# Kernel optimization log

Measured on AMD Instinct MI355X. Metric: run time of the kernel, lower is better.

## Reference

```python
import jax, jax.numpy as jnp
import numpy as np

B, OUT, IN = 2048, 4096, 4096
KEEPRATE = 0.5  # mid-training drop schedule state; first-call default masks nothing


def setup_inputs() -> dict:
    key = jax.random.key(0)
    k1, k2, k3, k4 = jax.random.split(key, 4)
    data = jax.random.normal(k1, (B, IN), dtype=jnp.float32)
    # weight parameter = fftn of a real N(0, 0.1) matrix, stored as complex
    w0 = jax.random.normal(k2, (OUT, IN), dtype=jnp.float32) * 0.1
    wc = jnp.fft.fftn(w0.astype(jnp.float32))
    w_real = jnp.real(wc).astype(jnp.float32)
    w_imag = jnp.imag(wc).astype(jnp.float32)
    bias = jax.random.normal(k3, (OUT,), dtype=jnp.float32) * 0.1
    # ZMAT: rank assignment, a permutation of 0..OUT*IN-1
    zmat = jax.random.permutation(k4, jnp.arange(OUT * IN, dtype=jnp.int64)).reshape(OUT, IN)
    return {"data": data, "w_real": w_real, "w_imag": w_imag, "bias": bias, "zmat": zmat}


def reference(data, w_real, w_imag, bias, zmat):
    O, I = w_real.shape
    numel = O * I
    threval = KEEPRATE * numel
    # IDROP: keep entries whose rank <= threshold (ZMAT > threval -> 0)
    idrop = (zmat.astype(jnp.float32) <= threval).astype(w_real.dtype)
    dropweight = (w_real + 1j * w_imag) * idrop  # masked FFT-domain weight
    # torch.fft.irfftn(dropweight, s=(O, I)): full ifft on dim 0, real irfft on dim 1
    # (numpy/jax irfft crops the last axis to I//2+1, same as torch)
    w_spatial = jnp.fft.irfftn(dropweight, s=(O, I), axes=(0, 1)).astype(data.dtype)
    return data @ w_spatial.T + bias
```

## Files before the change

### kernel.cpp

```cpp
#include <hip/hip_runtime.h>
#include <hip/hip_bf16.h>
#include <stdint.h>

#define OUT_N 4096
#define IN_N  4096
#define BATCH 2048
#define KHALF 2049

typedef __bf16 bf16x8 __attribute__((ext_vector_type(8)));
typedef float  f32x4  __attribute__((ext_vector_type(4)));

__device__ __forceinline__ unsigned short f2bf(float f) {
  unsigned int u = __builtin_bit_cast(unsigned int, f);
  u += 0x7FFFu + ((u >> 16) & 1u);
  return (unsigned short)(u >> 16);
}

__device__ __forceinline__ float2 cmul(float2 a, float2 b) {
  return make_float2(a.x * b.x - a.y * b.y, a.x * b.y + a.y * b.x);
}
__device__ __forceinline__ float2 cadd(float2 a, float2 b) { return make_float2(a.x + b.x, a.y + b.y); }
__device__ __forceinline__ float2 csub(float2 a, float2 b) { return make_float2(a.x - b.x, a.y - b.y); }
__device__ __forceinline__ float2 muli(float2 a) { return make_float2(-a.y, a.x); }

__device__ __forceinline__ void dft4i(float2& x0, float2& x1, float2& x2, float2& x3) {
  float2 t0 = cadd(x0, x2), t1 = csub(x0, x2);
  float2 t2 = cadd(x1, x3), t3 = csub(x1, x3);
  float2 it3 = muli(t3);
  x0 = cadd(t0, t2); x2 = csub(t0, t2);
  x1 = cadd(t1, it3); x3 = csub(t1, it3);
}

#define C8f  0.70710678118654752f
#define C16f 0.92387953251128676f
#define S16f 0.38268343236508977f

__device__ __forceinline__ void dft16i(float2 r[16]) {
  float2 t[16];
#pragma unroll
  for (int b = 0; b < 4; ++b) {
    float2 a0 = r[b], a1 = r[4 + b], a2 = r[8 + b], a3 = r[12 + b];
    dft4i(a0, a1, a2, a3);
    t[b * 4 + 0] = a0; t[b * 4 + 1] = a1; t[b * 4 + 2] = a2; t[b * 4 + 3] = a3;
  }
  const float2 W1 = make_float2(C16f, S16f);
  const float2 W2 = make_float2(C8f, C8f);
  const float2 W3 = make_float2(S16f, C16f);
  const float2 W6 = make_float2(-C8f, C8f);
  const float2 W9 = make_float2(-C16f, -S16f);
  t[5]  = cmul(t[5],  W1);  t[6]  = cmul(t[6],  W2);  t[7]  = cmul(t[7],  W3);
  t[9]  = cmul(t[9],  W2);  t[10] = muli(t[10]);      t[11] = cmul(t[11], W6);
  t[13] = cmul(t[13], W3);  t[14] = cmul(t[14], W6);  t[15] = cmul(t[15], W9);
#pragma unroll
  for (int q = 0; q < 4; ++q) {
    float2 a0 = t[q], a1 = t[4 + q], a2 = t[8 + q], a3 = t[12 + q];
    dft4i(a0, a1, a2, a3);
    r[q] = a0; r[q + 4] = a1; r[q + 8] = a2; r[q + 12] = a3;
  }
}

__device__ __forceinline__ void twiddle16(float2 r[16], float theta) {
  float sn, cs;
  __sincosf(theta, &sn, &cs);
  float2 w = make_float2(cs, sn);
  float2 wk = w;
  r[1] = cmul(r[1], wk);
#pragma unroll
  for (int k = 2; k < 16; ++k) {
    wk = cmul(wk, w);
    r[k] = cmul(r[k], wk);
  }
}

__device__ void fft4096_core(float2 r[16], float2* lds, int t) {
  dft16i(r);
  twiddle16(r, 1.53398078788564123e-3f * (float)t);
#pragma unroll
  for (int k1 = 0; k1 < 16; ++k1) lds[k1 * 257 + t] = r[k1];
  __syncthreads();
  const int k1 = t & 15, b = t >> 4;
  float2 s[16];
#pragma unroll
  for (int a = 0; a < 16; ++a) s[a] = lds[k1 * 257 + 16 * a + b];
  __syncthreads();
  dft16i(s);
  twiddle16(s, 2.45436926061702596e-2f * (float)b);
#pragma unroll
  for (int c = 0; c < 16; ++c) lds[k1 * 273 + c * 17 + b] = s[c];
  __syncthreads();
#pragma unroll
  for (int bb = 0; bb < 16; ++bb) r[bb] = lds[k1 * 273 + b * 17 + bb];
  dft16i(r);
}

__global__ void mask_transpose(const float* __restrict__ wr, const float* __restrict__ wi,
                               const int* __restrict__ zmat, float2* __restrict__ wt) {
  __shared__ float2 tile[32][33];
  const int k0 = blockIdx.x * 32;
  const int o0 = blockIdx.y * 32;
  const int tx = threadIdx.x;
  const int ty = threadIdx.y;
#pragma unroll
  for (int r = 0; r < 4; ++r) {
    int o = o0 + ty + r * 8;
    int k = k0 + tx;
    float2 v = make_float2(0.f, 0.f);
    if (k < KHALF) {
      size_t idx = (size_t)o * IN_N + k;
      if (zmat[idx] <= 8388608) v = make_float2(wr[idx], wi[idx]);
    }
    tile[ty + r * 8][tx] = v;
  }
  __syncthreads();
#pragma unroll
  for (int r = 0; r < 4; ++r) {
    int k = k0 + ty + r * 8;
    int o = o0 + tx;
    if (k < KHALF) wt[(size_t)k * OUT_N + o] = tile[tx][ty + r * 8];
  }
}

__global__ __launch_bounds__(256) void col_ifft(float2* __restrict__ wt) {
  __shared__ float2 lds[4368];
  const int t = threadIdx.x;
  float2* row = wt + (size_t)blockIdx.x * OUT_N;
  float2 r[16];
#pragma unroll
  for (int n1 = 0; n1 < 16; ++n1) r[n1] = row[n1 * 256 + t];
  fft4096_core(r, lds, t);
#pragma unroll
  for (int d = 0; d < 16; ++d) row[t + 256 * d] = r[d];
}

__global__ void transpose_ko(const float2* __restrict__ yt, float2* __restrict__ y) {
  __shared__ float2 tile[32][33];
  const int k0 = blockIdx.x * 32;
  const int o0 = blockIdx.y * 32;
  const int tx = threadIdx.x;
  const int ty = threadIdx.y;
#pragma unroll
  for (int r = 0; r < 4; ++r) {
    int k = k0 + ty + r * 8;
    int o = o0 + tx;
    if (k < KHALF) tile[ty + r * 8][tx] = yt[(size_t)k * OUT_N + o];
  }
  __syncthreads();
#pragma unroll
  for (int r = 0; r < 4; ++r) {
    int o = o0 + ty + r * 8;
    int k = k0 + tx;
    if (k < KHALF) y[(size_t)o * KHALF + k] = tile[tx][ty + r * 8];
  }
}

__global__ __launch_bounds__(256) void row_irfft(const float2* __restrict__ y,
                                                 unsigned short* __restrict__ wbf) {
  __shared__ float2 lds[4368];
  const int t = threadIdx.x;
  const float2* row = y + (size_t)blockIdx.x * KHALF;
#pragma unroll
  for (int j = 0; j < 9; ++j) {
    int k = t + j * 256;
    if (k < KHALF) lds[k] = row[k];
  }
  __syncthreads();
  float2 r[16];
#pragma unroll
  for (int n1 = 0; n1 < 16; ++n1) {
    int m = n1 * 256 + t;
    float2 v;
    if (m == 0)         v = make_float2(lds[0].x, 0.f);
    else if (m < 2048)  v = lds[m];
    else if (m == 2048) v = make_float2(lds[2048].x, 0.f);
    else { float2 u = lds[4096 - m]; v = make_float2(u.x, -u.y); }
    r[n1] = v;
  }
  __syncthreads();
  fft4096_core(r, lds, t);
  const float sc = 1.0f / (4096.0f * 4096.0f);
  unsigned short* orow = wbf + (size_t)blockIdx.x * IN_N;
#pragma unroll
  for (int d = 0; d < 16; ++d) orow[t + 256 * d] = f2bf(r[d].x * sc);
}

__global__ void cvt_bf16(const float* __restrict__ x, unsigned short* __restrict__ o, int n4) {
  int i = blockIdx.x * blockDim.x + threadIdx.x;
  if (i < n4) {
    float4 v = ((const float4*)x)[i];
    ushort4 r;
    r.x = f2bf(v.x); r.y = f2bf(v.y); r.z = f2bf(v.z); r.w = f2bf(v.w);
    ((ushort4*)o)[i] = r;
  }
}

__device__ __forceinline__ void gload_lds16(const void* gp, void* lp) {
  typedef const __attribute__((address_space(1))) void* gptr_t;
  typedef __attribute__((address_space(3))) void* lptr_t;
  __builtin_amdgcn_global_load_lds((gptr_t)(unsigned long long)gp,
                                   (lptr_t)(unsigned int)(unsigned long long)lp,
                                   16, 0, 0);
}

__global__ __launch_bounds__(256) void gemm_bt_bias(const unsigned short* __restrict__ A,
                                                    const unsigned short* __restrict__ B,
                                                    const float* __restrict__ bias,
                                                    float* __restrict__ C) {
  __shared__ __align__(16) unsigned short As[128 * 32];
  __shared__ __align__(16) unsigned short Bs[128 * 32];
  const int tid  = threadIdx.x;
  const int wave = tid >> 6;
  const int lane = tid & 63;
  const int gm0 = blockIdx.y * 128;
  const int gn0 = blockIdx.x * 128;

  f32x4 acc[4][4] = {};
  const int wm = wave >> 1, wn = wave & 1;
  const int lrow = lane >> 2;
  const int lcol = (lane & 3) * 8;

  for (int kt = 0; kt < IN_N; kt += 32) {
#pragma unroll
    for (int j = 0; j < 2; ++j) {
      const int rbase = wave * 32 + j * 16;
      gload_lds16(A + ((size_t)(gm0 + rbase + lrow) * IN_N + kt + lcol),
                  As + (size_t)rbase * 32);
      gload_lds16(B + ((size_t)(gn0 + rbase + lrow) * IN_N + kt + lcol),
                  Bs + (size_t)rbase * 32);
    }
    __syncthreads();

    bf16x8 af[4], bfr[4];
#pragma unroll
    for (int i = 0; i < 4; ++i) {
      af[i]  = *(const bf16x8*)&As[(wm * 64 + i * 16 + (lane & 15)) * 32 + (lane >> 4) * 8];
      bfr[i] = *(const bf16x8*)&Bs[(wn * 64 + i * 16 + (lane & 15)) * 32 + (lane >> 4) * 8];
    }
#pragma unroll
    for (int mi = 0; mi < 4; ++mi)
#pragma unroll
      for (int ni = 0; ni < 4; ++ni)
        acc[mi][ni] = __builtin_amdgcn_mfma_f32_16x16x32_bf16(af[mi], bfr[ni], acc[mi][ni], 0, 0, 0);
    __syncthreads();
  }

  const int col0 = gn0 + wn * 64 + (lane & 15);
  const int row0 = gm0 + wm * 64 + (lane >> 4) * 4;
#pragma unroll
  for (int mi = 0; mi < 4; ++mi) {
#pragma unroll
    for (int ni = 0; ni < 4; ++ni) {
      int col = col0 + ni * 16;
      float bv = bias[col];
#pragma unroll
      for (int r = 0; r < 4; ++r) {
        int row = row0 + mi * 16 + r;
        C[(size_t)row * OUT_N + col] = acc[mi][ni][r] + bv;
      }
    }
  }
}

extern "C" void kernel_launch(void* const* d_in, const int* in_sizes, int n_in,
                              void* d_out, int out_size, void* d_ws, size_t ws_size,
                              hipStream_t stream) {
  const float* data = (const float*)d_in[0];
  const float* wr   = (const float*)d_in[1];
  const float* wi   = (const float*)d_in[2];
  const float* bias = (const float*)d_in[3];
  const int*   zmat = (const int*)d_in[4];

  char* ws = (char*)d_ws;
  float2* wt = (float2*)ws;
  float2* y  = (float2*)(ws + 67141632ull);
  unsigned short* wbf = (unsigned short*)ws;
  unsigned short* dbf = (unsigned short*)(ws + 33554432ull);

  hipLaunchKernelGGL(mask_transpose, dim3(65, 128), dim3(32, 8), 0, stream, wr, wi, zmat, wt);
  hipLaunchKernelGGL(col_ifft,       dim3(2049),    dim3(256),   0, stream, wt);
  hipLaunchKernelGGL(transpose_ko,   dim3(65, 128), dim3(32, 8), 0, stream, wt, y);
  hipLaunchKernelGGL(row_irfft,      dim3(4096),    dim3(256),   0, stream, y, wbf);
  hipLaunchKernelGGL(cvt_bf16,       dim3(8192),    dim3(256),   0, stream, data, dbf, (BATCH * IN_N) / 4);
  hipLaunchKernelGGL(gemm_bt_bias,   dim3(OUT_N / 128, BATCH / 128), dim3(256), 0, stream,
                     dbf, wbf, bias, (float*)d_out);
}
```

Baseline: 376.9 us.

## Pack two real-output row IFFTs per complex FFT and use 8-wave GEMM blocks

The row inverse real FFT now handles two output rows per block. It packs them as a + i·b into one complex 4096-point FFT, so the real and imaginary parts of the result are the two spatial rows. This halves the number of FFT blocks and the FFT arithmetic for that stage. Separately, the GEMM block grows from 256 to 512 threads, with each of the 8 waves computing a 64x32 sub-tile instead of 64x64. The aim is more waves to hide latency, at the cost of lower per-wave register reuse, and more LDS reads per MFMA.

```diff
diff --git a/kernel.cpp b/kernel.cpp
--- a/kernel.cpp
+++ b/kernel.cpp
@@ -153,34 +153,43 @@
   }
 }
 
-__global__ __launch_bounds__(256) void row_irfft(const float2* __restrict__ y,
-                                                 unsigned short* __restrict__ wbf) {
+__global__ __launch_bounds__(256) void row_irfft2(const float2* __restrict__ y,
+                                                  unsigned short* __restrict__ wbf) {
   __shared__ float2 lds[4368];
   const int t = threadIdx.x;
-  const float2* row = y + (size_t)blockIdx.x * KHALF;
+  const int oa = blockIdx.x * 2, ob = oa + 1;
+  const float2* rowa = y + (size_t)oa * KHALF;
+  const float2* rowb = y + (size_t)ob * KHALF;
+  float2* lsa = lds;
+  float2* lsb = lds + 2049;
 #pragma unroll
   for (int j = 0; j < 9; ++j) {
     int k = t + j * 256;
-    if (k < KHALF) lds[k] = row[k];
+    if (k < KHALF) { lsa[k] = rowa[k]; lsb[k] = rowb[k]; }
   }
   __syncthreads();
   float2 r[16];
 #pragma unroll
   for (int n1 = 0; n1 < 16; ++n1) {
     int m = n1 * 256 + t;
-    float2 v;
-    if (m == 0)         v = make_float2(lds[0].x, 0.f);
-    else if (m < 2048)  v = lds[m];
-    else if (m == 2048) v = make_float2(lds[2048].x, 0.f);
-    else { float2 u = lds[4096 - m]; v = make_float2(u.x, -u.y); }
-    r[n1] = v;
+    float2 za, zb;
+    if (m == 0)        { za = make_float2(lsa[0].x, 0.f);    zb = make_float2(lsb[0].x, 0.f); }
+    else if (m < 2048) { za = lsa[m];                        zb = lsb[m]; }
+    else if (m == 2048){ za = make_float2(lsa[2048].x, 0.f); zb = make_float2(lsb[2048].x, 0.f); }
+    else { float2 ua = lsa[4096 - m], ub = lsb[4096 - m];
+           za = make_float2(ua.x, -ua.y); zb = make_float2(ub.x, -ub.y); }
+    r[n1] = make_float2(za.x - zb.y, za.y + zb.x);
   }
   __syncthreads();
   fft4096_core(r, lds, t);
   const float sc = 1.0f / (4096.0f * 4096.0f);
-  unsigned short* orow = wbf + (size_t)blockIdx.x * IN_N;
-#pragma unroll
-  for (int d = 0; d < 16; ++d) orow[t + 256 * d] = f2bf(r[d].x * sc);
+  unsigned short* orow_a = wbf + (size_t)oa * IN_N;
+  unsigned short* orow_b = wbf + (size_t)ob * IN_N;
+#pragma unroll
+  for (int d = 0; d < 16; ++d) {
+    orow_a[t + 256 * d] = f2bf(r[d].x * sc);
+    orow_b[t + 256 * d] = f2bf(r[d].y * sc);
+  }
 }
 
 __global__ void cvt_bf16(const float* __restrict__ x, unsigned short* __restrict__ o, int n4) {
@@ -201,7 +210,7 @@
                                    16, 0, 0);
 }
 
-__global__ __launch_bounds__(256) void gemm_bt_bias(const unsigned short* __restrict__ A,
+__global__ __launch_bounds__(512) void gemm_bt_bias(const unsigned short* __restrict__ A,
                                                     const unsigned short* __restrict__ B,
                                                     const float* __restrict__ bias,
                                                     float* __restrict__ C) {
@@ -213,42 +222,40 @@
   const int gm0 = blockIdx.y * 128;
   const int gn0 = blockIdx.x * 128;
 
-  f32x4 acc[4][4] = {};
-  const int wm = wave >> 1, wn = wave & 1;
+  f32x4 acc[4][2] = {};
+  const int wm = wave >> 2, wn = wave & 3;
   const int lrow = lane >> 2;
   const int lcol = (lane & 3) * 8;
+  const int rbase = wave * 16;
 
   for (int kt = 0; kt < IN_N; kt += 32) {
-#pragma unroll
-    for (int j = 0; j < 2; ++j) {
-      const int rbase = wave * 32 + j * 16;
-      gload_lds16(A + ((size_t)(gm0 + rbase + lrow) * IN_N + kt + lcol),
-                  As + (size_t)rbase * 32);
-      gload_lds16(B + ((size_t)(gn0 + rbase + lrow) * IN_N + kt + lcol),
-                  Bs + (size_t)rbase * 32);
-    }
+    gload_lds16(A + ((size_t)(gm0 + rbase + lrow) * IN_N + kt + lcol),
+                As + (size_t)rbase * 32);
+    gload_lds16(B + ((size_t)(gn0 + rbase + lrow) * IN_N + kt + lcol),
+                Bs + (size_t)rbase * 32);
     __syncthreads();
 
-    bf16x8 af[4], bfr[4];
-#pragma unroll
-    for (int i = 0; i < 4; ++i) {
+    bf16x8 af[4], bfr[2];
+#pragma unroll
+    for (int i = 0; i < 4; ++i)
       af[i]  = *(const bf16x8*)&As[(wm * 64 + i * 16 + (lane & 15)) * 32 + (lane >> 4) * 8];
-      bfr[i] = *(const bf16x8*)&Bs[(wn * 64 + i * 16 + (lane & 15)) * 32 + (lane >> 4) * 8];
-    }
+#pragma unroll
+    for (int j = 0; j < 2; ++j)
+      bfr[j] = *(const bf16x8*)&Bs[(wn * 32 + j * 16 + (lane & 15)) * 32 + (lane >> 4) * 8];
 #pragma unroll
     for (int mi = 0; mi < 4; ++mi)
 #pragma unroll
-      for (int ni = 0; ni < 4; ++ni)
+      for (int ni = 0; ni < 2; ++ni)
         acc[mi][ni] = __builtin_amdgcn_mfma_f32_16x16x32_bf16(af[mi], bfr[ni], acc[mi][ni], 0, 0, 0);
     __syncthreads();
   }
 
-  const int col0 = gn0 + wn * 64 + (lane & 15);
+  const int col0 = gn0 + wn * 32 + (lane & 15);
   const int row0 = gm0 + wm * 64 + (lane >> 4) * 4;
 #pragma unroll
   for (int mi = 0; mi < 4; ++mi) {
 #pragma unroll
-    for (int ni = 0; ni < 4; ++ni) {
+    for (int ni = 0; ni < 2; ++ni) {
       int col = col0 + ni * 16;
       float bv = bias[col];
 #pragma unroll
@@ -278,8 +285,8 @@
   hipLaunchKernelGGL(mask_transpose, dim3(65, 128), dim3(32, 8), 0, stream, wr, wi, zmat, wt);
   hipLaunchKernelGGL(col_ifft,       dim3(2049),    dim3(256),   0, stream, wt);
   hipLaunchKernelGGL(transpose_ko,   dim3(65, 128), dim3(32, 8), 0, stream, wt, y);
-  hipLaunchKernelGGL(row_irfft,      dim3(4096),    dim3(256),   0, stream, y, wbf);
+  hipLaunchKernelGGL(row_irfft2,     dim3(2048),    dim3(256),   0, stream, y, wbf);
   hipLaunchKernelGGL(cvt_bf16,       dim3(8192),    dim3(256),   0, stream, data, dbf, (BATCH * IN_N) / 4);
-  hipLaunchKernelGGL(gemm_bt_bias,   dim3(OUT_N / 128, BATCH / 128), dim3(256), 0, stream,
+  hipLaunchKernelGGL(gemm_bt_bias,   dim3(OUT_N / 128, BATCH / 128), dim3(512), 0, stream,
                      dbf, wbf, bias, (float*)d_out);
 }
```

After: 377.3 us. No clear change (+0.1%).
